# Kernel tuning notes

Measured on AMD Instinct MI355X. Metric: run time of the kernel, lower is better.

The kernel has to match this reference:

```python
import jax, jax.numpy as jnp
import numpy as np

N_HEADS = 8
OUT_FEATURES = 64
LEAKY_SLOPE = 0.2
MASK_FILL = -1e9


def setup_inputs() -> dict:
    key = jax.random.key(0)
    k_h, k_adj, k_W, k_a = jax.random.split(key, 4)
    B, N, F_IN = 1, 4096, 128
    h = jax.random.normal(k_h, (B, N, F_IN), dtype=jnp.float32)
    adj_mat = jax.random.randint(k_adj, (N, N), 0, 2, dtype=jnp.int32)
    # glorot-style scaled params
    W = jax.random.normal(k_W, (F_IN, OUT_FEATURES * N_HEADS), dtype=jnp.float32) * (1.0 / np.sqrt(F_IN))
    a = jax.random.normal(k_a, (N_HEADS, 2 * OUT_FEATURES, 1), dtype=jnp.float32) * (1.0 / np.sqrt(2 * OUT_FEATURES))
    return {"h": h, "adj_mat": adj_mat, "W": W, "a": a}


def reference(h, adj_mat, W, a):
    B, N, _ = h.shape
    heads = a.shape[0]
    out = a.shape[1] // 2
    # linear transform + head split (same reshape order as tf.reshape)
    ht = jnp.reshape(h @ W, (-1, heads, N, out))            # (B, heads, N, out)
    # additive attention scores
    src = jnp.einsum('bhnf,hfo->bhno', ht, a[:, :out, :])    # (B, heads, N, 1)
    tgt = jnp.einsum('bhnf,hfo->bhno', ht, a[:, out:, :])    # (B, heads, N, 1)
    e = src + jnp.swapaxes(tgt, -1, -2)                      # (B, heads, N, N)
    e = jnp.where(e > 0, e, LEAKY_SLOPE * e)                 # leaky_relu
    e = jnp.where(adj_mat > 0, e, MASK_FILL)                 # adjacency mask
    attention = jax.nn.softmax(e, axis=-1)
    h_prime = attention @ ht                                 # (B, heads, N, out)
    return h_prime
```

## Files before the change

### kernel.cpp

```cpp
#include <hip/hip_runtime.h>
#include <stdint.h>

#define HT_STRIDE 262144
#define LOG2E 1.4426950408889634f

typedef __attribute__((ext_vector_type(8))) short bf16x8;
typedef __attribute__((ext_vector_type(4))) float f32x4;
typedef __attribute__((ext_vector_type(2))) float f32x2;

__device__ __forceinline__ unsigned short f2bf(float f) {
    unsigned int u = __float_as_uint(f);
    u += 0x7FFFu + ((u >> 16) & 1u);
    return (unsigned short)(u >> 16);
}

__device__ __forceinline__ float exp2_fast(float e) {
#if __has_builtin(__builtin_amdgcn_exp2f)
    return __builtin_amdgcn_exp2f(e);
#else
    return __expf(e * 0.6931471805599453f);
#endif
}

__global__ void __launch_bounds__(256) k_fused(const float* __restrict__ h,
                                               const int* __restrict__ adj,
                                               const float* __restrict__ W,
                                               const float* __restrict__ aW,
                                               float* __restrict__ ess,
                                               float* __restrict__ ets,
                                               unsigned short* __restrict__ htT2,
                                               unsigned int* __restrict__ abm) {
    __shared__ unsigned int ldsT[1024];
    __shared__ float hs[8][128];
    __shared__ float ldsA[64][66];
    __shared__ float redS[4][64];
    __shared__ float redT[4][64];
    const int t = threadIdx.x;

    if (blockIdx.x < 512) {
        const int lane = t & 63;
        const int w = t >> 6;
        const int sb = blockIdx.x >> 3;
        const int cq = blockIdx.x & 7;
        for (int rr = 0; rr < 16; ++rr) {
            const int* arow = adj + (sb * 64 + w * 16 + rr) * 4096 + cq * 512;
            int v[8];
            #pragma unroll
            for (int j = 0; j < 8; ++j) v[j] = arow[j * 64 + lane];
            #pragma unroll
            for (int j = 0; j < 8; ++j) {
                unsigned long long m = __ballot(v[j] > 0);
                if (lane < 2)
                    ldsT[(2 * j + lane) * 64 + rr * 4 + w] = (unsigned int)(m >> (lane * 32));
            }
        }
        __syncthreads();
        ((uint4*)(abm + (sb * 128 + cq * 16) * 64))[t] = ((uint4*)ldsT)[t];
    } else {
        const int bid2 = (int)blockIdx.x - 512;
        const int n0 = bid2 * 8;
        const int p0 = bid2 * 64;
        const int hd = p0 >> 12;
        const int m0 = p0 & 4095;

        {
            float4 v = ((const float4*)(h + n0 * 128))[t];
            int e = t * 4;
            int r = e >> 7, f = e & 127;
            hs[r][f + 0] = v.x; hs[r][f + 1] = v.y;
            hs[r][f + 2] = v.z; hs[r][f + 3] = v.w;
        }
        __syncthreads();

        float acc0[8], acc1[8];
        #pragma unroll
        for (int r = 0; r < 8; ++r) { acc0[r] = 0.f; acc1[r] = 0.f; }
        const float2* Wf = (const float2*)W;
        for (int f = 0; f < 128; ++f) {
            float2 wp = Wf[f * 256 + t];
            #pragma unroll
            for (int r = 0; r < 8; ++r) {
                float hv = hs[r][f];
                acc0[r] = fmaf(hv, wp.x, acc0[r]);
                acc1[r] = fmaf(hv, wp.y, acc1[r]);
            }
        }
        {
            const int ns = t >> 5;
            const int o = (2 * t) & 63;
            #pragma unroll
            for (int r = 0; r < 8; ++r) {
                *(float2*)&ldsA[r * 8 + ns][o] = make_float2(acc0[r], acc1[r]);
            }
        }
        __syncthreads();

        {
            const int r = t & 63, og = t >> 6;
            float sdot = 0.f, gdot = 0.f;
            #pragma unroll
            for (int k = 0; k < 16; ++k) {
                int o = og * 16 + k;
                float hv = ldsA[r][o];
                sdot = fmaf(hv, aW[hd * 128 + o], sdot);
                gdot = fmaf(hv, aW[hd * 128 + 64 + o], gdot);
            }
            redS[og][r] = sdot; redT[og][r] = gdot;
        }
        __syncthreads();
        if (t < 64) {
            float sp = (redS[0][t] + redS[1][t] + redS[2][t] + redS[3][t]) * LOG2E;
            ess[hd * 8192 + m0 + t]        = exp2_fast(sp);
            ess[hd * 8192 + 4096 + m0 + t] = exp2_fast(0.2f * sp);
        } else if (t < 128) {
            int r = t - 64;
            float tv = (redT[0][r] + redT[1][r] + redT[2][r] + redT[3][r]) * LOG2E;
            ets[hd * 8192 + m0 + r]        = exp2_fast(tv);
            ets[hd * 8192 + 4096 + m0 + r] = exp2_fast(0.2f * tv);
        }

        unsigned short* d = htT2 + (hd * 128 + (m0 >> 5)) * 2048;
        #pragma unroll
        for (int i = 0; i < 16; ++i) {
            int id = t + 256 * i;
            int mi = id & 31, o = (id >> 5) & 63, ct = id >> 11;
            d[ct * 2048 + o * 32 + mi] = f2bf(ldsA[mi + 32 * ct][o]);
        }
    }
}

__global__ void __launch_bounds__(256, 4) k_attn(const unsigned int* __restrict__ abm,
                                                 const unsigned short* __restrict__ htT2,
                                                 const float* __restrict__ ess,
                                                 const float* __restrict__ ets,
                                                 float* __restrict__ out) {
    __shared__ __align__(16) float smem[8192];

    const int t = threadIdx.x;
    const int kq = t >> 6;
    const int lane = t & 63;
    const int li = lane & 15;
    const int quad = lane >> 4;
    const int head = blockIdx.x & 7;
    const int s32 = blockIdx.x >> 3;
    const int s64 = s32 >> 1, half = s32 & 1;
    const int i0 = s32 * 32;

    {
        const float4* esrc = (const float4*)(ets + head * 8192);
        float4* edst = (float4*)smem;
        #pragma unroll
        for (int i = 0; i < 8; ++i) edst[t + 256 * i] = esrc[t + 256 * i];
    }

    f32x2 esv[2], es2v[2];
    #pragma unroll
    for (int g2 = 0; g2 < 2; ++g2) {
        float e1 = ess[head * 8192 + i0 + 16 * g2 + li];
        float e2 = ess[head * 8192 + 4096 + i0 + 16 * g2 + li];
        esv[g2]  = (f32x2){e1, e1};
        es2v[g2] = (f32x2){e2, e2};
    }

    f32x4 acc[8];
    #pragma unroll
    for (int i = 0; i < 8; ++i) acc[i] = (f32x4){0.f, 0.f, 0.f, 0.f};
    f32x4 apd[2];
    apd[0] = (f32x4){0.f, 0.f, 0.f, 0.f};
    apd[1] = (f32x4){0.f, 0.f, 0.f, 0.f};

    const uint4 onesw = {0x3F803F80u, 0x3F803F80u, 0x3F803F80u, 0x3F803F80u};
    const bf16x8 aones = __builtin_bit_cast(bf16x8, onesw);

    const uint4* ap = (const uint4*)(htT2 + head * HT_STRIDE) + (li * 4 + quad);
    const unsigned int* bmp = abm + s64 * 8192 + half * 2 + li * 4;

    __syncthreads();

    const int c0 = kq * 32;
    #pragma unroll 1
    for (int ci = 0; ci < 32; ++ci) {
        const int c = c0 + ci;
        uint4 av0 = ap[c * 256 + 0];
        uint4 av1 = ap[c * 256 + 64];
        uint4 av2 = ap[c * 256 + 128];
        uint4 av3 = ap[c * 256 + 192];
        uint2 bw = *(const uint2*)(bmp + c * 64);

        const float4* etp  = (const float4*)(smem + c * 32 + quad * 8);
        const float4* et2p = (const float4*)(smem + 4096 + c * 32 + quad * 8);
        float4 ta = etp[0],  tb = etp[1];
        float4 ua = et2p[0], ub = et2p[1];
        const f32x2 etq[4]  = {(f32x2){ta.x, ta.y}, (f32x2){ta.z, ta.w},
                               (f32x2){tb.x, tb.y}, (f32x2){tb.z, tb.w}};
        const f32x2 et2q[4] = {(f32x2){ua.x, ua.y}, (f32x2){ua.z, ua.w},
                               (f32x2){ub.x, ub.y}, (f32x2){ub.z, ub.w}};

        const unsigned int wb[2] = {bw.x, bw.y};
        #pragma unroll
        for (int g2 = 0; g2 < 2; ++g2) {
            const unsigned int wq = wb[g2] >> (quad * 8);
            unsigned int pk[4];
            #pragma unroll
            for (int m = 0; m < 4; ++m) {
                f32x2 p1 = etq[m] * esv[g2];
                f32x2 p2 = et2q[m] * es2v[g2];
                float w0 = fmaxf(p1[0], p2[0]);
                float w1 = fmaxf(p1[1], p2[1]);
                unsigned int pkm;
                asm("v_cvt_pk_bf16_f32 %0, %1, %2" : "=v"(pkm) : "v"(w0), "v"(w1));
                const int j0 = 2 * m, j1 = 2 * m + 1;
                const unsigned int lo = (unsigned int)((int)(wq << (31 - j0)) >> 31);
                const unsigned int hi = (unsigned int)((int)(wq << (31 - j1)) >> 31);
                pk[m] = pkm & ((lo & 0x0000FFFFu) | (hi & 0xFFFF0000u));
            }
            uint4 bv; bv.x = pk[0]; bv.y = pk[1]; bv.z = pk[2]; bv.w = pk[3];
            bf16x8 bfrag = __builtin_bit_cast(bf16x8, bv);
            apd[g2] = __builtin_amdgcn_mfma_f32_16x16x32_bf16(aones, bfrag, apd[g2], 0, 0, 0);
            acc[g2 * 4 + 0] = __builtin_amdgcn_mfma_f32_16x16x32_bf16(__builtin_bit_cast(bf16x8, av0), bfrag, acc[g2 * 4 + 0], 0, 0, 0);
            acc[g2 * 4 + 1] = __builtin_amdgcn_mfma_f32_16x16x32_bf16(__builtin_bit_cast(bf16x8, av1), bfrag, acc[g2 * 4 + 1], 0, 0, 0);
            acc[g2 * 4 + 2] = __builtin_amdgcn_mfma_f32_16x16x32_bf16(__builtin_bit_cast(bf16x8, av2), bfrag, acc[g2 * 4 + 2], 0, 0, 0);
            acc[g2 * 4 + 3] = __builtin_amdgcn_mfma_f32_16x16x32_bf16(__builtin_bit_cast(bf16x8, av3), bfrag, acc[g2 * 4 + 3], 0, 0, 0);
        }
    }

    __syncthreads();
    if (kq != 0) {
        float* cb = smem + ((kq - 1) * 64 + lane) * 36;
        #pragma unroll
        for (int i = 0; i < 8; ++i) ((f32x4*)cb)[i] = acc[i];
        cb[32] = apd[0][0]; cb[33] = apd[1][0];
    }
    __syncthreads();
    if (kq == 0) {
        float pd[2] = {apd[0][0], apd[1][0]};
        #pragma unroll
        for (int q = 0; q < 3; ++q) {
            const float* cb = smem + (q * 64 + lane) * 36;
            #pragma unroll
            for (int i = 0; i < 8; ++i) acc[i] += ((const f32x4*)cb)[i];
            pd[0] += cb[32]; pd[1] += cb[33];
        }
        #pragma unroll
        for (int g2 = 0; g2 < 2; ++g2) {
            const float rd = 1.0f / pd[g2];
            float4* op = (float4*)(out + head * HT_STRIDE + (i0 + 16 * g2 + li) * 64);
            #pragma unroll
            for (int f = 0; f < 4; ++f) {
                f32x4 a = acc[g2 * 4 + f];
                op[f * 4 + quad] = make_float4(a[0] * rd, a[1] * rd, a[2] * rd, a[3] * rd);
            }
        }
    }
}

extern "C" void kernel_launch(void* const* d_in, const int* in_sizes, int n_in,
                              void* d_out, int out_size, void* d_ws, size_t ws_size,
                              hipStream_t stream) {
    const float* h   = (const float*)d_in[0];
    const int*   adj = (const int*)d_in[1];
    const float* W   = (const float*)d_in[2];
    const float* aW  = (const float*)d_in[3];
    float* out = (float*)d_out;

    char* ws = (char*)d_ws;
    float* ess = (float*)(ws);
    float* ets = (float*)(ws + 262144);
    unsigned int*   abm  = (unsigned int*)(ws + 524288);
    unsigned short* htT2 = (unsigned short*)(ws + 2621440);

    hipLaunchKernelGGL(k_fused, dim3(1024), dim3(256), 0, stream,
                       h, adj, W, aW, ess, ets, htT2, abm);
    hipLaunchKernelGGL(k_attn,  dim3(1024), dim3(256), 0, stream,
                       abm, htT2, ess, ets, out);
}
```

Baseline: 150.4 us.

## Interleave fused-kernel roles, prefetch W, and split attention key range across 8 waves

The prologue kernel now interleaves adjacency-bitmask blocks with projection blocks (even/odd block ids) rather than running them as two contiguous halves, so the two workloads mix across CUs. The projection loop software-prefetches the next four W rows into registers. The attention kernel doubles its block to 512 threads, giving each of 8 waves 16 key chunks instead of 32, and replaces the single-step partial-sum merge with a tree reduction through LDS. The larger block and enlarged LDS buffer may reduce occupancy, and the tree reduction adds extra barriers.

After: 401.7 us. +167.1%, slower.

```diff
diff --git a/kernel.cpp b/kernel.cpp
--- a/kernel.cpp
+++ b/kernel.cpp
@@ -37,11 +37,12 @@
     __shared__ float redT[4][64];
     const int t = threadIdx.x;
 
-    if (blockIdx.x < 512) {
+    if ((blockIdx.x & 1) == 0) {
+        const int eid = (int)blockIdx.x >> 1;
         const int lane = t & 63;
         const int w = t >> 6;
-        const int sb = blockIdx.x >> 3;
-        const int cq = blockIdx.x & 7;
+        const int sb = eid >> 3;
+        const int cq = eid & 7;
         for (int rr = 0; rr < 16; ++rr) {
             const int* arow = adj + (sb * 64 + w * 16 + rr) * 4096 + cq * 512;
             int v[8];
@@ -57,7 +58,7 @@
         __syncthreads();
         ((uint4*)(abm + (sb * 128 + cq * 16) * 64))[t] = ((uint4*)ldsT)[t];
     } else {
-        const int bid2 = (int)blockIdx.x - 512;
+        const int bid2 = (int)blockIdx.x >> 1;
         const int n0 = bid2 * 8;
         const int p0 = bid2 * 64;
         const int hd = p0 >> 12;
@@ -76,14 +77,26 @@
         #pragma unroll
         for (int r = 0; r < 8; ++r) { acc0[r] = 0.f; acc1[r] = 0.f; }
         const float2* Wf = (const float2*)W;
-        for (int f = 0; f < 128; ++f) {
-            float2 wp = Wf[f * 256 + t];
-            #pragma unroll
-            for (int r = 0; r < 8; ++r) {
-                float hv = hs[r][f];
-                acc0[r] = fmaf(hv, wp.x, acc0[r]);
-                acc1[r] = fmaf(hv, wp.y, acc1[r]);
-            }
+        float2 wpb[4];
+        #pragma unroll
+        for (int j = 0; j < 4; ++j) wpb[j] = Wf[j * 256 + t];
+        for (int fb = 0; fb < 32; ++fb) {
+            const int fn = ((fb + 1) & 31) * 4;
+            float2 wn[4];
+            #pragma unroll
+            for (int j = 0; j < 4; ++j) wn[j] = Wf[(fn + j) * 256 + t];
+            #pragma unroll
+            for (int j = 0; j < 4; ++j) {
+                const int f = fb * 4 + j;
+                #pragma unroll
+                for (int r = 0; r < 8; ++r) {
+                    float hv = hs[r][f];
+                    acc0[r] = fmaf(hv, wpb[j].x, acc0[r]);
+                    acc1[r] = fmaf(hv, wpb[j].y, acc1[r]);
+                }
+            }
+            #pragma unroll
+            for (int j = 0; j < 4; ++j) wpb[j] = wn[j];
         }
         {
             const int ns = t >> 5;
@@ -129,12 +142,12 @@
     }
 }
 
-__global__ void __launch_bounds__(256, 4) k_attn(const unsigned int* __restrict__ abm,
+__global__ void __launch_bounds__(512, 8) k_attn(const unsigned int* __restrict__ abm,
                                                  const unsigned short* __restrict__ htT2,
                                                  const float* __restrict__ ess,
                                                  const float* __restrict__ ets,
                                                  float* __restrict__ out) {
-    __shared__ __align__(16) float smem[8192];
+    __shared__ __align__(16) float smem[9216];
 
     const int t = threadIdx.x;
     const int kq = t >> 6;
@@ -150,7 +163,7 @@
         const float4* esrc = (const float4*)(ets + head * 8192);
         float4* edst = (float4*)smem;
         #pragma unroll
-        for (int i = 0; i < 8; ++i) edst[t + 256 * i] = esrc[t + 256 * i];
+        for (int i = 0; i < 4; ++i) edst[t + 512 * i] = esrc[t + 512 * i];
     }
 
     f32x2 esv[2], es2v[2];
@@ -177,9 +190,9 @@
 
     __syncthreads();
 
-    const int c0 = kq * 32;
+    const int c0 = kq * 16;
     #pragma unroll 1
-    for (int ci = 0; ci < 32; ++ci) {
+    for (int ci = 0; ci < 16; ++ci) {
         const int c = c0 + ci;
         uint4 av0 = ap[c * 256 + 0];
         uint4 av1 = ap[c * 256 + 64];
@@ -224,26 +237,52 @@
         }
     }
 
-    __syncthreads();
-    if (kq != 0) {
-        float* cb = smem + ((kq - 1) * 64 + lane) * 36;
+    float pdv[2] = {apd[0][0], apd[1][0]};
+    __syncthreads();
+
+    if (kq >= 4) {
+        float* cb = smem + ((kq - 4) * 64 + lane) * 36;
         #pragma unroll
         for (int i = 0; i < 8; ++i) ((f32x4*)cb)[i] = acc[i];
-        cb[32] = apd[0][0]; cb[33] = apd[1][0];
+        cb[32] = pdv[0]; cb[33] = pdv[1];
+    }
+    __syncthreads();
+    if (kq < 4) {
+        const float* cb = smem + (kq * 64 + lane) * 36;
+        #pragma unroll
+        for (int i = 0; i < 8; ++i) acc[i] += ((const f32x4*)cb)[i];
+        pdv[0] += cb[32]; pdv[1] += cb[33];
+    }
+    __syncthreads();
+    if (kq == 2 || kq == 3) {
+        float* cb = smem + ((kq - 2) * 64 + lane) * 36;
+        #pragma unroll
+        for (int i = 0; i < 8; ++i) ((f32x4*)cb)[i] = acc[i];
+        cb[32] = pdv[0]; cb[33] = pdv[1];
+    }
+    __syncthreads();
+    if (kq < 2) {
+        const float* cb = smem + (kq * 64 + lane) * 36;
+        #pragma unroll
+        for (int i = 0; i < 8; ++i) acc[i] += ((const f32x4*)cb)[i];
+        pdv[0] += cb[32]; pdv[1] += cb[33];
+    }
+    __syncthreads();
+    if (kq == 1) {
+        float* cb = smem + lane * 36;
+        #pragma unroll
+        for (int i = 0; i < 8; ++i) ((f32x4*)cb)[i] = acc[i];
+        cb[32] = pdv[0]; cb[33] = pdv[1];
     }
     __syncthreads();
     if (kq == 0) {
-        float pd[2] = {apd[0][0], apd[1][0]};
-        #pragma unroll
-        for (int q = 0; q < 3; ++q) {
-            const float* cb = smem + (q * 64 + lane) * 36;
-            #pragma unroll
-            for (int i = 0; i < 8; ++i) acc[i] += ((const f32x4*)cb)[i];
-            pd[0] += cb[32]; pd[1] += cb[33];
-        }
+        const float* cb = smem + lane * 36;
+        #pragma unroll
+        for (int i = 0; i < 8; ++i) acc[i] += ((const f32x4*)cb)[i];
+        pdv[0] += cb[32]; pdv[1] += cb[33];
         #pragma unroll
         for (int g2 = 0; g2 < 2; ++g2) {
-            const float rd = 1.0f / pd[g2];
+            const float rd = 1.0f / pdv[g2];
             float4* op = (float4*)(out + head * HT_STRIDE + (i0 + 16 * g2 + li) * 64);
             #pragma unroll
             for (int f = 0; f < 4; ++f) {
@@ -271,6 +310,6 @@
 
     hipLaunchKernelGGL(k_fused, dim3(1024), dim3(256), 0, stream,
                        h, adj, W, aW, ess, ets, htT2, abm);
-    hipLaunchKernelGGL(k_attn,  dim3(1024), dim3(256), 0, stream,
+    hipLaunchKernelGGL(k_attn,  dim3(1024), dim3(512), 0, stream,
                        abm, htT2, ess, ets, out);
 }
```
